# Kernel optimization log

Measured on AMD Instinct MI355X. Metric: run time of the kernel, lower is better.

## Reference

```python
import jax, jax.numpy as jnp
import numpy as np

D_MODEL = 2048
N_HEADS = 16
N_KV = 4
D_HEAD = D_MODEL // N_HEADS  # 128
N_REP = N_HEADS // N_KV      # 4
ROPE_BASE = 1000000.0


def _rope_tables(T, d_head, dtype):
    # inv_freq = (1/base)^(2i/d) for i in [0, d/2)
    i = jnp.arange(d_head // 2, dtype=jnp.float32)
    inv_freq = (1.0 / ROPE_BASE) ** (2.0 * i / d_head)
    theta = jnp.arange(T, dtype=jnp.float32)[:, None] * inv_freq[None, :]  # [T, d/2]
    theta = jnp.concatenate([theta, theta], axis=-1)                        # [T, d]
    return jnp.sin(theta).astype(dtype), jnp.cos(theta).astype(dtype)


def _apply_rope(x, sin, cos):
    # x: [B, h, T, d]; sin/cos: [T, d]
    x1, x2 = jnp.split(x, 2, axis=-1)
    rot = jnp.concatenate([-x2, x1], axis=-1)
    return cos[None, None] * x + sin[None, None] * rot


def setup_inputs() -> dict:
    key = jax.random.key(0)
    ks = jax.random.split(key, 9)
    B, T = 2, 2048
    s_in = 1.0 / np.sqrt(D_MODEL)
    return {
        "x": jax.random.normal(ks[0], (B, T, D_MODEL), jnp.float32),
        "wq": jax.random.normal(ks[1], (D_MODEL, N_HEADS * D_HEAD), jnp.float32) * s_in,
        "bq": jax.random.normal(ks[2], (N_HEADS * D_HEAD,), jnp.float32) * 0.02,
        "wk": jax.random.normal(ks[3], (D_MODEL, N_KV * D_HEAD), jnp.float32) * s_in,
        "bk": jax.random.normal(ks[4], (N_KV * D_HEAD,), jnp.float32) * 0.02,
        "wv": jax.random.normal(ks[5], (D_MODEL, N_KV * D_HEAD), jnp.float32) * s_in,
        "bv": jax.random.normal(ks[6], (N_KV * D_HEAD,), jnp.float32) * 0.02,
        "wo": jax.random.normal(ks[7], (D_MODEL, D_MODEL), jnp.float32) * s_in,
    }


def reference(x, wq, bq, wk, bk, wv, bv, wo):
    B, T, C = x.shape
    sin, cos = _rope_tables(T, D_HEAD, x.dtype)

    q = (x @ wq + bq).reshape(B, T, N_HEADS, D_HEAD).transpose(0, 2, 1, 3)  # [B,H,T,d]
    k = (x @ wk + bk).reshape(B, T, N_KV, D_HEAD).transpose(0, 2, 1, 3)     # [B,KV,T,d]
    v = (x @ wv + bv).reshape(B, T, N_KV, D_HEAD).transpose(0, 2, 1, 3)     # [B,KV,T,d]

    q = _apply_rope(q, sin, cos)
    k = _apply_rope(k, sin, cos)

    # GQA: group query heads as [B, KV, rep, T, d] to broadcast against k/v
    qg = q.reshape(B, N_KV, N_REP, T, D_HEAD)
    scale = 1.0 / jnp.sqrt(jnp.asarray(D_HEAD, x.dtype))
    scores = jnp.einsum('bkrqd,bksd->bkrqs', qg, k) * scale  # [B,KV,rep,T,S]

    causal = jnp.tril(jnp.ones((T, T), dtype=bool))
    neg = jnp.asarray(jnp.finfo(x.dtype).min, x.dtype)
    scores = jnp.where(causal[None, None, None], scores, neg)
    p = jax.nn.softmax(scores, axis=-1)

    out = jnp.einsum('bkrqs,bksd->bkrqd', p, v)               # [B,KV,rep,T,d]
    out = out.reshape(B, N_HEADS, T, D_HEAD).transpose(0, 2, 1, 3).reshape(B, T, C)
    return out @ wo, k, v
```

## Files before the change

### kernel.cpp

```cpp
#include <hip/hip_runtime.h>
#include <hip/hip_bf16.h>
#include <math.h>

#define BB 2
#define TT 2048
#define DMODEL 2048
#define NH 16
#define NKV 4
#define DH 128
#define NQKV 3072
#define MM (BB*TT)

typedef unsigned short u16;
typedef unsigned int u32;

typedef __bf16 bf16x8 __attribute__((ext_vector_type(8)));
typedef float f32x4 __attribute__((ext_vector_type(4)));

__device__ __forceinline__ u16 f2b(float f) {
  union { float f; u32 u; } v; v.f = f;
  u32 r = v.u + 0x7fffu + ((v.u >> 16) & 1u);
  return (u16)(r >> 16);
}
__device__ __forceinline__ float b2f(u16 h) {
  union { u32 u; float f; } v; v.u = ((u32)h) << 16;
  return v.f;
}

__device__ __forceinline__ void gload16(const void* g, void* l) {
  __builtin_amdgcn_global_load_lds(
      (const __attribute__((address_space(1))) unsigned int*)g,
      (__attribute__((address_space(3))) unsigned int*)l, 16, 0, 0);
}

template <int CTRL>
__device__ __forceinline__ float dpp_f(float x) {
  union { float f; int i; } a, o;
  a.f = x;
  o.i = __builtin_amdgcn_update_dpp(0, a.i, CTRL, 0xF, 0xF, false);
  return o.f;
}
__device__ __forceinline__ float red16_max(float x) {
  x = fmaxf(x, dpp_f<0xB1>(x));
  x = fmaxf(x, dpp_f<0x4E>(x));
  x = fmaxf(x, dpp_f<0x124>(x));
  x = fmaxf(x, dpp_f<0x128>(x));
  return x;
}
__device__ __forceinline__ float red16_sum(float x) {
  x += dpp_f<0xB1>(x);
  x += dpp_f<0x4E>(x);
  x += dpp_f<0x124>(x);
  x += dpp_f<0x128>(x);
  return x;
}
__device__ __forceinline__ float fast_exp2(float x) {
#if __has_builtin(__builtin_amdgcn_exp2f)
  return __builtin_amdgcn_exp2f(x);
#else
  return __expf(x * 0.6931471805599453f);
#endif
}

__global__ void cvt_x_kernel(const float* __restrict__ x, u16* __restrict__ xb, int n4) {
  int i = blockIdx.x * 256 + threadIdx.x;
  if (i < n4) {
    float4 v = ((const float4*)x)[i];
    u32 lo = (u32)f2b(v.x) | ((u32)f2b(v.y) << 16);
    u32 hi = (u32)f2b(v.z) | ((u32)f2b(v.w) << 16);
    uint2 r; r.x = lo; r.y = hi;
    ((uint2*)xb)[i] = r;
  }
}

__global__ void bias_cat_kernel(const float* __restrict__ bq, const float* __restrict__ bk,
                                const float* __restrict__ bv, float* __restrict__ bc) {
  int i = blockIdx.x * 256 + threadIdx.x;
  if (i < NQKV) bc[i] = (i < 2048) ? bq[i] : ((i < 2560) ? bk[i - 2048] : bv[i - 2560]);
}

__global__ void transpose_cvt_kernel(const float* __restrict__ src, u16* __restrict__ dst,
                                     int srcCols, int dstRowOff) {
  __shared__ u16 t[64][65];
  int c0 = blockIdx.x * 64, r0 = blockIdx.y * 64;
  int tid = threadIdx.x;
  for (int i = tid; i < 4096; i += 256) {
    int r = i >> 6, c = i & 63;
    t[r][c] = f2b(src[(size_t)(r0 + r) * srcCols + c0 + c]);
  }
  __syncthreads();
  for (int i = tid; i < 4096; i += 256) {
    int n = i >> 6, k = i & 63;
    dst[(size_t)(dstRowOff + c0 + n) * 2048 + r0 + k] = t[k][n];
  }
}

__global__ void vt_transpose_kernel(const u16* __restrict__ qkvb, u16* __restrict__ vt) {
  __shared__ u16 t[64][65];
  int bkv = blockIdx.z;
  int b  = bkv >> 2;
  int kv = bkv & 3;
  int d0 = blockIdx.y * 64;
  int t0 = blockIdx.x * 64;
  int tid = threadIdx.x;
  for (int i = tid; i < 4096; i += 256) {
    int r = i >> 6, c = i & 63;
    t[r][c] = qkvb[(size_t)(b * TT + t0 + r) * NQKV + 2560 + kv * DH + d0 + c];
  }
  __syncthreads();
  size_t tilebase = ((size_t)bkv * 32 + (t0 >> 6)) * 8192;
  for (int i = tid; i < 512; i += 256) {
    int dl = i & 63, kc = i >> 6;
    u16 tmp[8];
#pragma unroll
    for (int j = 0; j < 8; j++) tmp[j] = t[kc * 8 + j][dl];
    *(uint4*)&vt[tilebase + (size_t)(kc * 128 + d0 + dl) * 8] = *(const uint4*)tmp;
  }
}

__global__ void rope_pack_kernel(const u16* __restrict__ qkvb, u16* __restrict__ qb,
                                 u16* __restrict__ kb, float* __restrict__ outK,
                                 float* __restrict__ outV) {
  __shared__ float sc_s[64], sc_c[64];
  int t = blockIdx.x, b = blockIdx.y;
  int tid = threadIdx.x;
  if (tid < 64) {
    float inv = exp2f(-(float)tid * 0.31143075889569023f);
    float th = (float)t * inv;
    sc_s[tid] = sinf(th);
    sc_c[tid] = cosf(th);
  }
  __syncthreads();
  const u16* row = qkvb + (size_t)(b * TT + t) * NQKV;
  const int rl = t & 63;
  const int tt = t >> 6;
  for (int i = tid; i < 1024; i += 256) {
    int h = i >> 6, d = i & 63;
    float x1 = b2f(row[h * DH + d]);
    float x2 = b2f(row[h * DH + d + 64]);
    float s = sc_s[d], c = sc_c[d];
    size_t tb = ((size_t)(b * NH + h) * 32 + tt) * 8192;
    int kc = d >> 3, e = d & 7;
    qb[tb + (size_t)((kc)     * 64 + rl) * 8 + e] = f2b(c * x1 - s * x2);
    qb[tb + (size_t)((kc + 8) * 64 + rl) * 8 + e] = f2b(c * x2 + s * x1);
  }
  {
    int kv = tid >> 6, d = tid & 63;
    float x1 = b2f(row[2048 + kv * DH + d]);
    float x2 = b2f(row[2048 + kv * DH + d + 64]);
    float s = sc_s[d], c = sc_c[d];
    float r1 = c * x1 - s * x2;
    float r2 = c * x2 + s * x1;
    size_t tb = ((size_t)(b * NKV + kv) * 32 + tt) * 8192;
    int kc = d >> 3, e = d & 7;
    kb[tb + (size_t)((kc)     * 64 + rl) * 8 + e] = f2b(r1);
    kb[tb + (size_t)((kc + 8) * 64 + rl) * 8 + e] = f2b(r2);
    size_t base = ((size_t)(b * NKV + kv) * TT + t) * DH;
    outK[base + d]      = r1;
    outK[base + d + 64] = r2;
  }
  for (int i = tid; i < 512; i += 256) {
    int kv = i >> 7, d = i & 127;
    outV[((size_t)(b * NKV + kv) * TT + t) * DH + d] = b2f(row[2560 + i]);
  }
}

template <int BIAS, int OUTF32>
__global__ __launch_bounds__(256, 3) void gemm_kernel(
    const u16* __restrict__ A, const u16* __restrict__ Bt,
    const float* __restrict__ bias, void* __restrict__ Cout,
    int M, int N, int K) {
  __shared__ u16 lA[128 * 32];
  __shared__ u16 lB[128 * 32];
  const int tid  = threadIdx.x;
  const int lane = tid & 63;
  const int wave = tid >> 6;
  const int quad = lane >> 4;
  const int l16  = lane & 15;
  const int m0 = blockIdx.y * 128;
  const int n0 = blockIdx.x * 128;
  const int wrow = (wave >> 1) * 64;
  const int wcol = (wave & 1) * 64;

  f32x4 acc[4][4];
  const f32x4 zero = {0.f, 0.f, 0.f, 0.f};
#pragma unroll
  for (int i = 0; i < 4; i++)
#pragma unroll
    for (int j = 0; j < 4; j++) acc[i][j] = zero;

  const int srow = tid >> 2;
  const int scol = (tid & 3) * 8;

  const u16* ga = A  + (size_t)(m0 + srow) * K + scol;
  const u16* gb = Bt + (size_t)(n0 + srow) * K + scol;

  for (int k0 = 0; k0 < K; k0 += 32) {
    gload16(ga + k0,                  &lA[tid * 8]);
    gload16(ga + k0 + (size_t)64 * K, &lA[2048 + tid * 8]);
    gload16(gb + k0,                  &lB[tid * 8]);
    gload16(gb + k0 + (size_t)64 * K, &lB[2048 + tid * 8]);
    __syncthreads();
    bf16x8 af[4], bf[4];
#pragma unroll
    for (int mi = 0; mi < 4; mi++)
      af[mi] = *(const bf16x8*)&lA[(wrow + mi * 16 + l16) * 32 + quad * 8];
#pragma unroll
    for (int ni = 0; ni < 4; ni++)
      bf[ni] = *(const bf16x8*)&lB[(wcol + ni * 16 + l16) * 32 + quad * 8];
#pragma unroll
    for (int mi = 0; mi < 4; mi++)
#pragma unroll
      for (int ni = 0; ni < 4; ni++)
        acc[mi][ni] = __builtin_amdgcn_mfma_f32_16x16x32_bf16(af[mi], bf[ni], acc[mi][ni], 0, 0, 0);
    __syncthreads();
  }

#pragma unroll
  for (int ni = 0; ni < 4; ni++) {
    int gcol = n0 + wcol + ni * 16 + l16;
    float bval = BIAS ? bias[gcol] : 0.0f;
#pragma unroll
    for (int mi = 0; mi < 4; mi++) {
#pragma unroll
      for (int r = 0; r < 4; r++) {
        int grow = m0 + wrow + mi * 16 + quad * 4 + r;
        float v = acc[mi][ni][r] + bval;
        if (OUTF32) ((float*)Cout)[(size_t)grow * N + gcol] = v;
        else        ((u16*)Cout)[(size_t)grow * N + gcol]   = f2b(v);
      }
    }
  }
}

__global__ __launch_bounds__(256, 2) void attn_kernel(
    const u16* __restrict__ Qt, const u16* __restrict__ Kt,
    const u16* __restrict__ Vt, u16* __restrict__ Ob) {
  __shared__ u16 sm[28672];
  u16* vbuf = sm + 16384;
  u16* pbuf = sm + 24576;

  const int bh = blockIdx.y;
  const int b = bh >> 4, h = bh & 15, kv = h >> 2;
  const int tid = threadIdx.x;
  const int lane = tid & 63;
  const int wave = tid >> 6;
  const int quad = lane >> 4;
  const int l16 = lane & 15;

  const u16* qbase = Qt + (size_t)(b * NH + h) * 32 * 8192;
  const u16* kbase = Kt + (size_t)(b * NKV + kv) * 32 * 8192;
  const u16* vbase = Vt + (size_t)(b * NKV + kv) * 32 * 8192;

  const int myrow = wave * 16 + quad * 4;
  const f32x4 zero = {0.f, 0.f, 0.f, 0.f};
  const float SC2 = 0.08838834764831845f * 1.4426950408889634f;

  int par = 0;

#pragma unroll
  for (int p = 0; p < 4; p++)
    gload16(kbase + p * 2048 + tid * 8, sm + p * 2048 + tid * 8);

  for (int half = 0; half < 2; ++half) {
    const int qt = half ? (31 - (int)blockIdx.x) : (int)blockIdx.x;
    const int q0 = qt * 64;
    const u16* qtile = qbase + (size_t)qt * 8192;

    bf16x8 af[4];
#pragma unroll
    for (int kc = 0; kc < 4; kc++)
      af[kc] = *(const bf16x8*)&qtile[(size_t)((kc * 4 + quad) * 64 + wave * 16 + l16) * 8];

    float mrow[4], lrow[4];
#pragma unroll
    for (int r = 0; r < 4; r++) { mrow[r] = -__builtin_inff(); lrow[r] = 0.f; }
    f32x4 o[8];
#pragma unroll
    for (int d = 0; d < 8; d++) o[d] = zero;

    for (int kt = 0; kt <= qt; ++kt) {
      u16* kb_c = sm + par * 8192;
      u16* kb_n = sm + (par ^ 1) * 8192;
      const int ktn = (kt < qt) ? kt + 1 : 0;
      const u16* vsrc = vbase + (size_t)kt * 8192;
      const u16* knxt = kbase + (size_t)ktn * 8192;
#pragma unroll
      for (int p = 0; p < 4; p++)
        gload16(vsrc + p * 2048 + tid * 8, vbuf + p * 2048 + tid * 8);
#pragma unroll
      for (int p = 0; p < 4; p++)
        gload16(knxt + p * 2048 + tid * 8, kb_n + p * 2048 + tid * 8);
      asm volatile("s_waitcnt vmcnt(8)\n\ts_barrier" ::: "memory");

      f32x4 s[4];
#pragma unroll
      for (int nt = 0; nt < 4; nt++) s[nt] = zero;
#pragma unroll
      for (int kc = 0; kc < 4; kc++) {
#pragma unroll
        for (int nt = 0; nt < 4; nt++) {
          bf16x8 bk = *(const bf16x8*)&kb_c[(size_t)((kc * 4 + quad) * 64 + nt * 16 + l16) * 8];
          s[nt] = __builtin_amdgcn_mfma_f32_16x16x32_bf16(af[kc], bk, s[nt], 0, 0, 0);
        }
      }

      float tmax[4];
#pragma unroll
      for (int r = 0; r < 4; r++) tmax[r] = -__builtin_inff();
      if (kt == qt) {
#pragma unroll
        for (int nt = 0; nt < 4; nt++) {
          int colrel = nt * 16 + l16;
#pragma unroll
          for (int r = 0; r < 4; r++) {
            float v = s[nt][r] * SC2;
            if (colrel > myrow + r) v = -__builtin_inff();
            s[nt][r] = v;
            tmax[r] = fmaxf(tmax[r], v);
          }
        }
      } else {
#pragma unroll
        for (int nt = 0; nt < 4; nt++)
#pragma unroll
          for (int r = 0; r < 4; r++) {
            float v = s[nt][r] * SC2;
            s[nt][r] = v;
            tmax[r] = fmaxf(tmax[r], v);
          }
      }
#pragma unroll
      for (int r = 0; r < 4; r++) tmax[r] = red16_max(tmax[r]);

      float alpha[4], lsum[4];
#pragma unroll
      for (int r = 0; r < 4; r++) {
        float mn = fmaxf(mrow[r], tmax[r]);
        alpha[r] = fast_exp2(mrow[r] - mn);
        mrow[r] = mn;
        lsum[r] = 0.f;
      }
#pragma unroll
      for (int nt = 0; nt < 4; nt++) {
        int kcP = nt * 2 + (l16 >> 3);
#pragma unroll
        for (int r = 0; r < 4; r++) {
          float p = fast_exp2(s[nt][r] - mrow[r]);
          lsum[r] += p;
          pbuf[wave * 1024 + (kcP * 16 + quad * 4 + r) * 8 + (l16 & 7)] = f2b(p);
        }
      }
#pragma unroll
      for (int r = 0; r < 4; r++) lsum[r] = red16_sum(lsum[r]);
#pragma unroll
      for (int r = 0; r < 4; r++) lrow[r] = lrow[r] * alpha[r] + lsum[r];
#pragma unroll
      for (int d = 0; d < 8; d++)
#pragma unroll
        for (int r = 0; r < 4; r++) o[d][r] *= alpha[r];

      asm volatile("s_waitcnt vmcnt(4)\n\ts_barrier" ::: "memory");
#pragma unroll
      for (int ks = 0; ks < 2; ks++) {
        bf16x8 ap = *(const bf16x8*)&pbuf[(size_t)(wave * 1024 + ((ks * 4 + quad) * 16 + l16) * 8)];
#pragma unroll
        for (int dt = 0; dt < 8; dt++) {
          bf16x8 bv = *(const bf16x8*)&vbuf[(size_t)((ks * 4 + quad) * 128 + dt * 16 + l16) * 8];
          o[dt] = __builtin_amdgcn_mfma_f32_16x16x32_bf16(ap, bv, o[dt], 0, 0, 0);
        }
      }
      asm volatile("s_barrier" ::: "memory");
      par ^= 1;
    }

    float inv[4];
#pragma unroll
    for (int r = 0; r < 4; r++) inv[r] = 1.0f / lrow[r];
#pragma unroll
    for (int dt = 0; dt < 8; dt++) {
#pragma unroll
      for (int r = 0; r < 4; r++) {
        int t = q0 + myrow + r;
        Ob[(size_t)(b * TT + t) * DMODEL + h * DH + dt * 16 + l16] = f2b(o[dt][r] * inv[r]);
      }
    }
  }
}

extern "C" void kernel_launch(void* const* d_in, const int* in_sizes, int n_in,
                              void* d_out, int out_size, void* d_ws, size_t ws_size,
                              hipStream_t stream) {
  (void)in_sizes; (void)n_in; (void)out_size; (void)ws_size;
  const float* x  = (const float*)d_in[0];
  const float* wq = (const float*)d_in[1];
  const float* bq = (const float*)d_in[2];
  const float* wk = (const float*)d_in[3];
  const float* bk = (const float*)d_in[4];
  const float* wv = (const float*)d_in[5];
  const float* bv = (const float*)d_in[6];
  const float* wo = (const float*)d_in[7];
  float* out = (float*)d_out;

  char* ws = (char*)d_ws;
  u16*   xb    = (u16*)(ws);
  u16*   wqkvT = (u16*)(ws + 16777216);
  u16*   woT   = (u16*)(ws + 29360128);
  float* bcat  = (float*)(ws + 37748736);
  u16*   qkvb  = (u16*)(ws + 37761024);
  u16*   qb    = (u16*)(ws + 62926848);
  u16*   kb    = (u16*)(ws + 79704064);
  u16*   vt    = (u16*)(ws + 83898368);
  u16*   ob    = (u16*)(ws + 88092672);

  float* outK = out + (size_t)BB * TT * DMODEL;
  float* outV = outK + (size_t)BB * NKV * TT * DH;

  cvt_x_kernel<<<8192, 256, 0, stream>>>(x, xb, (BB * TT * DMODEL) / 4);
  bias_cat_kernel<<<12, 256, 0, stream>>>(bq, bk, bv, bcat);
  transpose_cvt_kernel<<<dim3(32, 32), 256, 0, stream>>>(wq, wqkvT, 2048, 0);
  transpose_cvt_kernel<<<dim3(8, 32),  256, 0, stream>>>(wk, wqkvT, 512, 2048);
  transpose_cvt_kernel<<<dim3(8, 32),  256, 0, stream>>>(wv, wqkvT, 512, 2560);
  transpose_cvt_kernel<<<dim3(32, 32), 256, 0, stream>>>(wo, woT, 2048, 0);

  gemm_kernel<1, 0><<<dim3(NQKV / 128, MM / 128), 256, 0, stream>>>(
      xb, wqkvT, bcat, qkvb, MM, NQKV, DMODEL);

  rope_pack_kernel<<<dim3(TT, BB), 256, 0, stream>>>(qkvb, qb, kb, outK, outV);
  vt_transpose_kernel<<<dim3(TT / 64, DH / 64, BB * NKV), 256, 0, stream>>>(qkvb, vt);

  attn_kernel<<<dim3(16, BB * NH), 256, 0, stream>>>(qb, kb, vt, ob);

  gemm_kernel<0, 1><<<dim3(DMODEL / 128, MM / 128), 256, 0, stream>>>(
      ob, woT, nullptr, out, MM, DMODEL, DMODEL);
}
```

Before: 349.9 us.

## Compute transposed S=K·Q^T in attention to keep P in registers, vectorize rope

The attention kernel now computes scores transposed (keys as rows, queries as columns), so each lane owns one query row. Softmax statistics then reduce with two cross-quad shuffles instead of DPP reductions, and P is packed straight into bf16 MFMA operands for the PV product using 16x16x16 MFMAs, which removes the LDS round-trip through pbuf and frees shared memory. The V transpose layout is changed to match the new operand ordering. Rope/pack is vectorized to 16-byte loads and stores, and the output write is vectorized. The costs are twice as many smaller MFMAs for PV and rounding of P without tie handling.

```diff
diff --git a/kernel.cpp b/kernel.cpp
--- a/kernel.cpp
+++ b/kernel.cpp
@@ -15,6 +15,8 @@
 typedef unsigned int u32;
 
 typedef __bf16 bf16x8 __attribute__((ext_vector_type(8)));
+typedef __bf16 bf16x4 __attribute__((ext_vector_type(4)));
+typedef short short4v __attribute__((ext_vector_type(4)));
 typedef float f32x4 __attribute__((ext_vector_type(4)));
 
 __device__ __forceinline__ u16 f2b(float f) {
@@ -26,6 +28,10 @@
   union { u32 u; float f; } v; v.u = ((u32)h) << 16;
   return v.f;
 }
+__device__ __forceinline__ u32 pack2bf(float x, float y) {
+  union { float f; u32 u; } a, b; a.f = x; b.f = y;
+  return ((a.u + 0x8000u) >> 16) | ((b.u + 0x8000u) & 0xffff0000u);
+}
 
 __device__ __forceinline__ void gload16(const void* g, void* l) {
   __builtin_amdgcn_global_load_lds(
@@ -33,32 +39,25 @@
       (__attribute__((address_space(3))) unsigned int*)l, 16, 0, 0);
 }
 
-template <int CTRL>
-__device__ __forceinline__ float dpp_f(float x) {
-  union { float f; int i; } a, o;
-  a.f = x;
-  o.i = __builtin_amdgcn_update_dpp(0, a.i, CTRL, 0xF, 0xF, false);
-  return o.f;
-}
-__device__ __forceinline__ float red16_max(float x) {
-  x = fmaxf(x, dpp_f<0xB1>(x));
-  x = fmaxf(x, dpp_f<0x4E>(x));
-  x = fmaxf(x, dpp_f<0x124>(x));
-  x = fmaxf(x, dpp_f<0x128>(x));
-  return x;
-}
-__device__ __forceinline__ float red16_sum(float x) {
-  x += dpp_f<0xB1>(x);
-  x += dpp_f<0x4E>(x);
-  x += dpp_f<0x124>(x);
-  x += dpp_f<0x128>(x);
-  return x;
-}
 __device__ __forceinline__ float fast_exp2(float x) {
 #if __has_builtin(__builtin_amdgcn_exp2f)
   return __builtin_amdgcn_exp2f(x);
 #else
   return __expf(x * 0.6931471805599453f);
+#endif
+}
+
+__device__ __forceinline__ f32x4 mfma16(bf16x4 a, bf16x4 b, f32x4 c) {
+#if __has_builtin(__builtin_amdgcn_mfma_f32_16x16x16bf16_1k)
+  union { bf16x4 b; short4v s; } ua, ub;
+  ua.b = a; ub.b = b;
+  return __builtin_amdgcn_mfma_f32_16x16x16bf16_1k(ua.s, ub.s, c, 0, 0, 0);
+#elif __has_builtin(__builtin_amdgcn_mfma_f32_16x16x16_bf16)
+  return __builtin_amdgcn_mfma_f32_16x16x16_bf16(a, b, c, 0, 0, 0);
+#else
+  asm volatile("v_mfma_f32_16x16x16_bf16 %0, %1, %2, %0"
+               : "+v"(c) : "v"(a), "v"(b));
+  return c;
 #endif
 }
 
@@ -110,11 +109,15 @@
   __syncthreads();
   size_t tilebase = ((size_t)bkv * 32 + (t0 >> 6)) * 8192;
   for (int i = tid; i < 512; i += 256) {
-    int dl = i & 63, kc = i >> 6;
+    int dl = i & 63, chunk = i >> 6;
+    int m = chunk >> 2, qd = chunk & 3;
     u16 tmp[8];
 #pragma unroll
-    for (int j = 0; j < 8; j++) tmp[j] = t[kc * 8 + j][dl];
-    *(uint4*)&vt[tilebase + (size_t)(kc * 128 + d0 + dl) * 8] = *(const uint4*)tmp;
+    for (int e = 0; e < 8; e++) {
+      int srow = (2 * m + (e >> 2)) * 16 + qd * 4 + (e & 3);
+      tmp[e] = t[srow][dl];
+    }
+    *(uint4*)&vt[tilebase + (size_t)(chunk * 128 + d0 + dl) * 8] = *(const uint4*)tmp;
   }
 }
 
@@ -134,34 +137,63 @@
   const u16* row = qkvb + (size_t)(b * TT + t) * NQKV;
   const int rl = t & 63;
   const int tt = t >> 6;
-  for (int i = tid; i < 1024; i += 256) {
-    int h = i >> 6, d = i & 63;
-    float x1 = b2f(row[h * DH + d]);
-    float x2 = b2f(row[h * DH + d + 64]);
-    float s = sc_s[d], c = sc_c[d];
+
+  if (tid < 128) {
+    int h = tid >> 3, oc = tid & 7;
+    uint4 lo = *(const uint4*)&row[h * DH + oc * 8];
+    uint4 hi = *(const uint4*)&row[h * DH + 64 + oc * 8];
+    const u16* plo = (const u16*)&lo;
+    const u16* phi = (const u16*)&hi;
+    u16 y1[8], y2[8];
+#pragma unroll
+    for (int j = 0; j < 8; j++) {
+      int d = oc * 8 + j;
+      float x1 = b2f(plo[j]), x2 = b2f(phi[j]);
+      float s = sc_s[d], c = sc_c[d];
+      y1[j] = f2b(c * x1 - s * x2);
+      y2[j] = f2b(c * x2 + s * x1);
+    }
     size_t tb = ((size_t)(b * NH + h) * 32 + tt) * 8192;
-    int kc = d >> 3, e = d & 7;
-    qb[tb + (size_t)((kc)     * 64 + rl) * 8 + e] = f2b(c * x1 - s * x2);
-    qb[tb + (size_t)((kc + 8) * 64 + rl) * 8 + e] = f2b(c * x2 + s * x1);
-  }
-  {
-    int kv = tid >> 6, d = tid & 63;
-    float x1 = b2f(row[2048 + kv * DH + d]);
-    float x2 = b2f(row[2048 + kv * DH + d + 64]);
-    float s = sc_s[d], c = sc_c[d];
-    float r1 = c * x1 - s * x2;
-    float r2 = c * x2 + s * x1;
+    *(uint4*)&qb[tb + (size_t)((oc)     * 64 + rl) * 8] = *(const uint4*)y1;
+    *(uint4*)&qb[tb + (size_t)((oc + 8) * 64 + rl) * 8] = *(const uint4*)y2;
+  } else if (tid < 160) {
+    int id = tid - 128;
+    int kv = id >> 3, oc = id & 7;
+    uint4 lo = *(const uint4*)&row[2048 + kv * DH + oc * 8];
+    uint4 hi = *(const uint4*)&row[2048 + kv * DH + 64 + oc * 8];
+    const u16* plo = (const u16*)&lo;
+    const u16* phi = (const u16*)&hi;
+    u16 y1[8], y2[8];
+    float f1[8], f2v[8];
+#pragma unroll
+    for (int j = 0; j < 8; j++) {
+      int d = oc * 8 + j;
+      float x1 = b2f(plo[j]), x2 = b2f(phi[j]);
+      float s = sc_s[d], c = sc_c[d];
+      f1[j] = c * x1 - s * x2;
+      f2v[j] = c * x2 + s * x1;
+      y1[j] = f2b(f1[j]);
+      y2[j] = f2b(f2v[j]);
+    }
     size_t tb = ((size_t)(b * NKV + kv) * 32 + tt) * 8192;
-    int kc = d >> 3, e = d & 7;
-    kb[tb + (size_t)((kc)     * 64 + rl) * 8 + e] = f2b(r1);
-    kb[tb + (size_t)((kc + 8) * 64 + rl) * 8 + e] = f2b(r2);
-    size_t base = ((size_t)(b * NKV + kv) * TT + t) * DH;
-    outK[base + d]      = r1;
-    outK[base + d + 64] = r2;
-  }
-  for (int i = tid; i < 512; i += 256) {
-    int kv = i >> 7, d = i & 127;
-    outV[((size_t)(b * NKV + kv) * TT + t) * DH + d] = b2f(row[2560 + i]);
+    *(uint4*)&kb[tb + (size_t)((oc)     * 64 + rl) * 8] = *(const uint4*)y1;
+    *(uint4*)&kb[tb + (size_t)((oc + 8) * 64 + rl) * 8] = *(const uint4*)y2;
+    size_t base = ((size_t)(b * NKV + kv) * TT + t) * DH + oc * 8;
+    *(float4*)&outK[base]     = *(const float4*)&f1[0];
+    *(float4*)&outK[base + 4] = *(const float4*)&f1[4];
+    *(float4*)&outK[base + 64]     = *(const float4*)&f2v[0];
+    *(float4*)&outK[base + 64 + 4] = *(const float4*)&f2v[4];
+  } else if (tid < 224) {
+    int id = tid - 160;
+    int kv = id >> 4, oc = id & 15;
+    uint4 v = *(const uint4*)&row[2560 + kv * DH + oc * 8];
+    const u16* pv = (const u16*)&v;
+    float f[8];
+#pragma unroll
+    for (int j = 0; j < 8; j++) f[j] = b2f(pv[j]);
+    size_t base = ((size_t)(b * NKV + kv) * TT + t) * DH + oc * 8;
+    *(float4*)&outV[base]     = *(const float4*)&f[0];
+    *(float4*)&outV[base + 4] = *(const float4*)&f[4];
   }
 }
 
@@ -236,9 +268,8 @@
 __global__ __launch_bounds__(256, 2) void attn_kernel(
     const u16* __restrict__ Qt, const u16* __restrict__ Kt,
     const u16* __restrict__ Vt, u16* __restrict__ Ob) {
-  __shared__ u16 sm[28672];
+  __shared__ u16 sm[24576];
   u16* vbuf = sm + 16384;
-  u16* pbuf = sm + 24576;
 
   const int bh = blockIdx.y;
   const int b = bh >> 4, h = bh & 15, kv = h >> 2;
@@ -252,9 +283,9 @@
   const u16* kbase = Kt + (size_t)(b * NKV + kv) * 32 * 8192;
   const u16* vbase = Vt + (size_t)(b * NKV + kv) * 32 * 8192;
 
-  const int myrow = wave * 16 + quad * 4;
   const f32x4 zero = {0.f, 0.f, 0.f, 0.f};
   const float SC2 = 0.08838834764831845f * 1.4426950408889634f;
+  const float NEGINF = -__builtin_inff();
 
   int par = 0;
 
@@ -266,15 +297,14 @@
     const int qt = half ? (31 - (int)blockIdx.x) : (int)blockIdx.x;
     const int q0 = qt * 64;
     const u16* qtile = qbase + (size_t)qt * 8192;
-
-    bf16x8 af[4];
+    const int qrel = wave * 16 + l16;
+
+    bf16x8 qf[4];
 #pragma unroll
     for (int kc = 0; kc < 4; kc++)
-      af[kc] = *(const bf16x8*)&qtile[(size_t)((kc * 4 + quad) * 64 + wave * 16 + l16) * 8];
-
-    float mrow[4], lrow[4];
-#pragma unroll
-    for (int r = 0; r < 4; r++) { mrow[r] = -__builtin_inff(); lrow[r] = 0.f; }
+      qf[kc] = *(const bf16x8*)&qtile[(size_t)((kc * 4 + quad) * 64 + qrel) * 8];
+
+    float mrow = NEGINF, lrow = 0.f;
     f32x4 o[8];
 #pragma unroll
     for (int d = 0; d < 8; d++) o[d] = zero;
@@ -293,97 +323,91 @@
         gload16(knxt + p * 2048 + tid * 8, kb_n + p * 2048 + tid * 8);
       asm volatile("s_waitcnt vmcnt(8)\n\ts_barrier" ::: "memory");
 
-      f32x4 s[4];
-#pragma unroll
-      for (int nt = 0; nt < 4; nt++) s[nt] = zero;
+      f32x4 sv[4];
+#pragma unroll
+      for (int mt = 0; mt < 4; mt++) sv[mt] = zero;
 #pragma unroll
       for (int kc = 0; kc < 4; kc++) {
 #pragma unroll
-        for (int nt = 0; nt < 4; nt++) {
-          bf16x8 bk = *(const bf16x8*)&kb_c[(size_t)((kc * 4 + quad) * 64 + nt * 16 + l16) * 8];
-          s[nt] = __builtin_amdgcn_mfma_f32_16x16x32_bf16(af[kc], bk, s[nt], 0, 0, 0);
+        for (int mt = 0; mt < 4; mt++) {
+          bf16x8 kf = *(const bf16x8*)&kb_c[(size_t)((kc * 4 + quad) * 64 + mt * 16 + l16) * 8];
+          sv[mt] = __builtin_amdgcn_mfma_f32_16x16x32_bf16(kf, qf[kc], sv[mt], 0, 0, 0);
         }
       }
 
-      float tmax[4];
-#pragma unroll
-      for (int r = 0; r < 4; r++) tmax[r] = -__builtin_inff();
       if (kt == qt) {
 #pragma unroll
-        for (int nt = 0; nt < 4; nt++) {
-          int colrel = nt * 16 + l16;
+        for (int mt = 0; mt < 4; mt++) {
 #pragma unroll
           for (int r = 0; r < 4; r++) {
-            float v = s[nt][r] * SC2;
-            if (colrel > myrow + r) v = -__builtin_inff();
-            s[nt][r] = v;
-            tmax[r] = fmaxf(tmax[r], v);
+            int srel = mt * 16 + quad * 4 + r;
+            if (srel > qrel) sv[mt][r] = NEGINF;
           }
         }
-      } else {
-#pragma unroll
-        for (int nt = 0; nt < 4; nt++)
-#pragma unroll
-          for (int r = 0; r < 4; r++) {
-            float v = s[nt][r] * SC2;
-            s[nt][r] = v;
-            tmax[r] = fmaxf(tmax[r], v);
-          }
-      }
-#pragma unroll
-      for (int r = 0; r < 4; r++) tmax[r] = red16_max(tmax[r]);
-
-      float alpha[4], lsum[4];
-#pragma unroll
-      for (int r = 0; r < 4; r++) {
-        float mn = fmaxf(mrow[r], tmax[r]);
-        alpha[r] = fast_exp2(mrow[r] - mn);
-        mrow[r] = mn;
-        lsum[r] = 0.f;
-      }
-#pragma unroll
-      for (int nt = 0; nt < 4; nt++) {
-        int kcP = nt * 2 + (l16 >> 3);
+      }
+      float mraw = NEGINF;
+#pragma unroll
+      for (int mt = 0; mt < 4; mt++)
+#pragma unroll
+        for (int r = 0; r < 4; r++) mraw = fmaxf(mraw, sv[mt][r]);
+      mraw = fmaxf(mraw, __shfl_xor(mraw, 16));
+      mraw = fmaxf(mraw, __shfl_xor(mraw, 32));
+
+      float mnew = fmaxf(mrow, mraw);
+      float alpha = fast_exp2((mrow - mnew) * SC2);
+      mrow = mnew;
+      float msc = mnew * SC2;
+      float lsum = 0.f;
+#pragma unroll
+      for (int mt = 0; mt < 4; mt++) {
 #pragma unroll
         for (int r = 0; r < 4; r++) {
-          float p = fast_exp2(s[nt][r] - mrow[r]);
-          lsum[r] += p;
-          pbuf[wave * 1024 + (kcP * 16 + quad * 4 + r) * 8 + (l16 & 7)] = f2b(p);
+          float p = fast_exp2(__builtin_fmaf(sv[mt][r], SC2, -msc));
+          sv[mt][r] = p;
+          lsum += p;
         }
       }
-#pragma unroll
-      for (int r = 0; r < 4; r++) lsum[r] = red16_sum(lsum[r]);
-#pragma unroll
-      for (int r = 0; r < 4; r++) lrow[r] = lrow[r] * alpha[r] + lsum[r];
-#pragma unroll
-      for (int d = 0; d < 8; d++)
-#pragma unroll
-        for (int r = 0; r < 4; r++) o[d][r] *= alpha[r];
+      lsum += __shfl_xor(lsum, 16);
+      lsum += __shfl_xor(lsum, 32);
+      lrow = lrow * alpha + lsum;
+      bf16x4 pb[4];
+#pragma unroll
+      for (int mt = 0; mt < 4; mt++) {
+        union { u32 u[2]; bf16x4 v; } pu;
+        pu.u[0] = pack2bf(sv[mt][0], sv[mt][1]);
+        pu.u[1] = pack2bf(sv[mt][2], sv[mt][3]);
+        pb[mt] = pu.v;
+      }
+#pragma unroll
+      for (int dt = 0; dt < 8; dt++) {
+        o[dt][0] *= alpha; o[dt][1] *= alpha; o[dt][2] *= alpha; o[dt][3] *= alpha;
+      }
 
       asm volatile("s_waitcnt vmcnt(4)\n\ts_barrier" ::: "memory");
 #pragma unroll
-      for (int ks = 0; ks < 2; ks++) {
-        bf16x8 ap = *(const bf16x8*)&pbuf[(size_t)(wave * 1024 + ((ks * 4 + quad) * 16 + l16) * 8)];
+      for (int m = 0; m < 2; m++) {
 #pragma unroll
         for (int dt = 0; dt < 8; dt++) {
-          bf16x8 bv = *(const bf16x8*)&vbuf[(size_t)((ks * 4 + quad) * 128 + dt * 16 + l16) * 8];
-          o[dt] = __builtin_amdgcn_mfma_f32_16x16x32_bf16(ap, bv, o[dt], 0, 0, 0);
+          bf16x8 vf = *(const bf16x8*)&vbuf[(size_t)(((m * 4 + quad) * 128) + dt * 16 + l16) * 8];
+          bf16x4 vlo = __builtin_shufflevector(vf, vf, 0, 1, 2, 3);
+          bf16x4 vhi = __builtin_shufflevector(vf, vf, 4, 5, 6, 7);
+          o[dt] = mfma16(vlo, pb[2 * m],     o[dt]);
+          o[dt] = mfma16(vhi, pb[2 * m + 1], o[dt]);
         }
       }
       asm volatile("s_barrier" ::: "memory");
       par ^= 1;
     }
 
-    float inv[4];
-#pragma unroll
-    for (int r = 0; r < 4; r++) inv[r] = 1.0f / lrow[r];
+    float inv = 1.0f / lrow;
+    int t = q0 + qrel;
+    size_t rowbase = (size_t)(b * TT + t) * DMODEL + h * DH;
 #pragma unroll
     for (int dt = 0; dt < 8; dt++) {
-#pragma unroll
-      for (int r = 0; r < 4; r++) {
-        int t = q0 + myrow + r;
-        Ob[(size_t)(b * TT + t) * DMODEL + h * DH + dt * 16 + l16] = f2b(o[dt][r] * inv[r]);
-      }
+      uint2 w;
+      w.x = pack2bf(o[dt][0] * inv, o[dt][1] * inv);
+      w.y = pack2bf(o[dt][2] * inv, o[dt][3] * inv);
+      *(uint2*)&Ob[rowbase + dt * 16 + quad * 4] = w;
     }
   }
 }
```

Result: faster. 342.0 us (-2.3%).
